# Performance work log

Hardware: AMD Instinct MI355X
Metric: run time of the kernel (lower is better)

The kernel has to match this reference:

```python
import jax, jax.numpy as jnp
import numpy as np

QK_DIM = 64
V_DIM = 64
NUM_Q_HEADS = 16
NUM_KV_HEADS = 4
GROUP = NUM_Q_HEADS // NUM_KV_HEADS
SCALE = 1.0 / (QK_DIM ** 0.5)


def setup_inputs() -> dict:
    key = jax.random.key(0)
    kq, kk, kv = jax.random.split(key, 3)
    B, S = 2, 2048
    Q = jax.random.normal(kq, (B, S, NUM_Q_HEADS * QK_DIM), dtype=jnp.float32)
    K = jax.random.normal(kk, (B, S, NUM_KV_HEADS * QK_DIM), dtype=jnp.float32)
    V = jax.random.normal(kv, (B, S, NUM_KV_HEADS * V_DIM), dtype=jnp.float32)
    # causal mask, [B, 1, S, S]; 0 entries are masked (matches masked_fill(mask == 0, -inf))
    mask = jnp.broadcast_to(jnp.tril(jnp.ones((S, S), dtype=jnp.int32))[None, None], (B, 1, S, S))
    return {"Q": Q, "K": K, "V": V, "mask": mask}


def reference(Q, K, V, mask):
    B, S, _ = Q.shape
    # [B, Hkv, g, S, d]
    Qg = Q.reshape(B, S, NUM_Q_HEADS, QK_DIM).transpose(0, 2, 1, 3).reshape(B, NUM_KV_HEADS, GROUP, S, QK_DIM)
    Kh = K.reshape(B, S, NUM_KV_HEADS, QK_DIM).transpose(0, 2, 1, 3)  # [B, Hkv, S, d]
    Vh = V.reshape(B, S, NUM_KV_HEADS, V_DIM).transpose(0, 2, 1, 3)   # [B, Hkv, S, dv]
    # scores: [B, Hkv, g, S, S]
    scores = jnp.einsum('bhgsd,bhtd->bhgst', Qg, Kh) * SCALE
    scores = jnp.where(mask[:, None] == 0, -jnp.inf, scores)
    probs = jax.nn.softmax(scores, axis=-1)
    # dropout p=0.0 -> identity (eval semantics)
    out = jnp.einsum('bhgst,bhtv->bhgsv', probs, Vh)
    return out
```

## Files before the change

### kernel.cpp

```cpp
#include <hip/hip_runtime.h>
#include <hip/hip_bf16.h>

typedef unsigned short u16;
typedef unsigned int u32;
typedef __attribute__((ext_vector_type(8))) short bf16x8;
typedef __attribute__((ext_vector_type(16))) float f32x16;

#define S_LEN 2048
#define NHQ   16
#define NHKV  4
#define HD    64
#define KVSTR (NHKV*HD)
#define QSTR  (NHQ*HD)
#define TILE_U16 4096
#define HEAD_U16 (32*TILE_U16)
#define VT_OFF   (8*HEAD_U16)
#define QSCALE 0.18033688011112042f
#define MBIAS (-24.0f)

__device__ __forceinline__ u32 cvt2(float lo, float hi) {
    __hip_bfloat162 hh = __float22bfloat162_rn(make_float2(lo, hi));
    union { __hip_bfloat162 h; u32 u; } c; c.h = hh; return c.u;
}
__device__ __forceinline__ u16 cvt1(float x) {
    __hip_bfloat16 hh = __float2bfloat16(x);
    union { __hip_bfloat16 h; u16 u; } c; c.h = hh; return c.u;
}

typedef __attribute__((address_space(3))) u32 lds_u32;
typedef __attribute__((address_space(1))) const u32 glb_u32;
__device__ __forceinline__ void gld_lds16(const void* g, void* l) {
    __builtin_amdgcn_global_load_lds((glb_u32*)g, (lds_u32*)l, 16, 0, 0);
}

__global__ __launch_bounds__(256)
void prep_kv(const float* __restrict__ Kp, const float* __restrict__ Vp,
             u16* __restrict__ WS)
{
    const int bid = blockIdx.x;
    const int t   = bid & 31;
    const int kvh = (bid >> 5) & 3;
    const int b   = bid >> 7;
    const int tid = threadIdx.x;

    u16* kt = WS + (size_t)bid * TILE_U16;
    u16* vt = WS + VT_OFF + (size_t)bid * TILE_U16;

    {
        const int r   = tid >> 2;
        const int c16 = (tid & 3) << 4;
        const float* kg = Kp + ((size_t)(b*S_LEN) + t*64 + r) * KVSTR + kvh*HD + c16;
        const float4 a  = *(const float4*)(kg);
        const float4 b4 = *(const float4*)(kg + 4);
        const float4 c  = *(const float4*)(kg + 8);
        const float4 d  = *(const float4*)(kg + 12);
        const int swz = (r & 7) << 3;
        *(uint4*)(kt + r*64 + (c16 ^ swz)) =
            make_uint4(cvt2(a.x,a.y), cvt2(a.z,a.w), cvt2(b4.x,b4.y), cvt2(b4.z,b4.w));
        *(uint4*)(kt + r*64 + ((c16+8) ^ swz)) =
            make_uint4(cvt2(c.x,c.y), cvt2(c.z,c.w), cvt2(d.x,d.y), cvt2(d.z,d.w));
    }
    {
        const int kv  = tid & 63;
        const int dv0 = (tid >> 6) << 4;
        const float* vg = Vp + ((size_t)(b*S_LEN) + t*64 + kv) * KVSTR + kvh*HD + dv0;
        float4 vv[4];
        vv[0] = *(const float4*)(vg);
        vv[1] = *(const float4*)(vg + 4);
        vv[2] = *(const float4*)(vg + 8);
        vv[3] = *(const float4*)(vg + 12);
        #pragma unroll
        for (int g4 = 0; g4 < 4; ++g4) {
            const int dv = dv0 + g4*4;
            vt[(dv+0)*64 + (kv ^ (((dv+0)&7)<<3))] = cvt1(vv[g4].x);
            vt[(dv+1)*64 + (kv ^ (((dv+1)&7)<<3))] = cvt1(vv[g4].y);
            vt[(dv+2)*64 + (kv ^ (((dv+2)&7)<<3))] = cvt1(vv[g4].z);
            vt[(dv+3)*64 + (kv ^ (((dv+3)&7)<<3))] = cvt1(vv[g4].w);
        }
    }
}

__global__ __launch_bounds__(512, 4)
void gqa_fwd_kernel(const float* __restrict__ Qp, const u16* __restrict__ WS,
                    float* __restrict__ Op)
{
    __shared__ __align__(16) char smem[65536];
    float* Mo = (float*)smem;
    float* Ml = (float*)(smem + 34816);

    const int tid  = threadIdx.x;
    const int w    = tid >> 6;
    const int lane = tid & 63;
    const int q31  = lane & 31;
    const int h    = lane >> 5;

    const int g  = __popc(w) & 1;
    const int rg = w >> 1;
    const int dr = rg >> 1;

    const int bid  = blockIdx.x;
    const int head = bid & 31;
    const int j    = bid >> 5;
    const int qt   = (j < 8) ? (15 - j) : (j - 8);
    const int kvh  = head & 3;
    const int b    = (head >> 2) & 1;
    const int qh   = kvh * 4 + (head >> 3);

    const u16* Kt = WS + (size_t)(b*4 + kvh) * HEAD_U16;
    const u16* Vt = WS + VT_OFF + (size_t)(b*4 + kvh) * HEAD_U16;

    const int qrow = qt*128 + rg*32 + q31;
    const int qcmp = (rg & 1)*32 + q31;
    const float* qp = Qp + ((size_t)b * S_LEN + qrow) * QSTR + qh*HD;
    float*       ob = Op + ((size_t)(b*NHQ + qh) * S_LEN + qrow) * HD;

    const size_t gofs = (size_t)rg*2048 + (size_t)lane*16;

    const int rswz = (q31 & 7) << 3;

    {
        const char* kg = (const char*)(Kt + (size_t)g*TILE_U16) + gofs;
        const char* vg = (const char*)(Vt + (size_t)g*TILE_U16) + gofs;
        char* kl = smem + (g*2 + 0)*8192 + rg*2048;
        char* vl = smem + 32768 + (g*2 + 0)*8192 + rg*2048;
        gld_lds16(kg, kl);  gld_lds16(kg + 1024, kl + 1024);
        gld_lds16(vg, vl);  gld_lds16(vg + 1024, vl + 1024);
    }

    bf16x8 qf[4];
    #pragma unroll
    for (int ks = 0; ks < 4; ++ks) {
        const int d = ks*16 + h*8;
        const float4 x = *(const float4*)(qp + d);
        const float4 y = *(const float4*)(qp + d + 4);
        union { u32 u[4]; bf16x8 v; } t4;
        t4.u[0] = cvt2(x.x*QSCALE, x.y*QSCALE);
        t4.u[1] = cvt2(x.z*QSCALE, x.w*QSCALE);
        t4.u[2] = cvt2(y.x*QSCALE, y.y*QSCALE);
        t4.u[3] = cvt2(y.z*QSCALE, y.w*QSCALE);
        qf[ks] = t4.v;
    }

    f32x16 MB;
    #pragma unroll
    for (int i = 0; i < 16; ++i) MB[i] = MBIAS;

    f32x16 oacc0, oacc1;
    #pragma unroll
    for (int i = 0; i < 16; ++i) { oacc0[i] = 0.f; oacc1[i] = 0.f; }
    float l_p = 0.f;

    __syncthreads();

    for (int p = 0; p <= qt; ++p) {
        const int bf = p & 1;
        if (p < qt) {
            const char* kg = (const char*)(Kt + (size_t)(2*(p+1)+g)*TILE_U16) + gofs;
            const char* vg = (const char*)(Vt + (size_t)(2*(p+1)+g)*TILE_U16) + gofs;
            char* kl = smem + (g*2 + (bf^1))*8192 + rg*2048;
            char* vl = smem + 32768 + (g*2 + (bf^1))*8192 + rg*2048;
            gld_lds16(kg, kl);  gld_lds16(kg + 1024, kl + 1024);
            gld_lds16(vg, vl);  gld_lds16(vg + 1024, vl + 1024);
        }

        if (p < qt || !(dr == 0 && g == 1)) {
            const u16* Kb = (const u16*)(smem + (g*2 + bf)*8192);
            const u16* Vb = (const u16*)(smem + 32768 + (g*2 + bf)*8192);

            f32x16 s0, s1;
            __builtin_amdgcn_s_setprio(1);
            {
                const int col = (h*8) ^ rswz;
                bf16x8 k0 = *(const bf16x8*)(&Kb[q31*64 + col]);
                bf16x8 k1 = *(const bf16x8*)(&Kb[(32 + q31)*64 + col]);
                s0 = __builtin_amdgcn_mfma_f32_32x32x16_bf16(k0, qf[0], MB, 0, 0, 0);
                s1 = __builtin_amdgcn_mfma_f32_32x32x16_bf16(k1, qf[0], MB, 0, 0, 0);
            }
            #pragma unroll
            for (int ks = 1; ks < 4; ++ks) {
                const int col = (ks*16 + h*8) ^ rswz;
                bf16x8 k0 = *(const bf16x8*)(&Kb[q31*64 + col]);
                bf16x8 k1 = *(const bf16x8*)(&Kb[(32 + q31)*64 + col]);
                s0 = __builtin_amdgcn_mfma_f32_32x32x16_bf16(k0, qf[ks], s0, 0, 0, 0);
                s1 = __builtin_amdgcn_mfma_f32_32x32x16_bf16(k1, qf[ks], s1, 0, 0, 0);
            }
            __builtin_amdgcn_s_setprio(0);

            if (p == qt && g == dr) {
                #pragma unroll
                for (int r = 0; r < 16; ++r) {
                    const int kvl = (r & 3) + 8*(r >> 2) + 4*h;
                    if (kvl > qcmp)      s0[r] = -1e30f;
                    if (kvl + 32 > qcmp) s1[r] = -1e30f;
                }
            }

            float ps0 = 0.f, ps1 = 0.f;
            #pragma unroll
            for (int r = 0; r < 16; ++r) {
                const float p0 = __builtin_amdgcn_exp2f(s0[r]);
                const float p1 = __builtin_amdgcn_exp2f(s1[r]);
                s0[r] = p0; ps0 += p0;
                s1[r] = p1; ps1 += p1;
            }
            l_p += ps0 + ps1;

            u32 Aw[8], Bw[8];
            #pragma unroll
            for (int m = 0; m < 4; ++m) {
                Aw[m]   = cvt2(s0[m*4+0], s0[m*4+1]);
                Bw[m]   = cvt2(s0[m*4+2], s0[m*4+3]);
                Aw[4+m] = cvt2(s1[m*4+0], s1[m*4+1]);
                Bw[4+m] = cvt2(s1[m*4+2], s1[m*4+3]);
            }

            __builtin_amdgcn_s_setprio(1);
            #pragma unroll
            for (int c = 0; c < 4; ++c) {
                u32 w0 = Aw[2*c], w2 = Aw[2*c+1];
                u32 w1 = Bw[2*c], w3 = Bw[2*c+1];
                asm("v_permlane32_swap_b32 %0, %1" : "+v"(w0), "+v"(w2));
                asm("v_permlane32_swap_b32 %0, %1" : "+v"(w1), "+v"(w3));
                union { u32 u[4]; bf16x8 v; } pu;
                pu.u[0] = w0; pu.u[1] = w1; pu.u[2] = w2; pu.u[3] = w3;
                const int col = (c*16 + h*8) ^ rswz;
                bf16x8 v0 = *(const bf16x8*)(&Vb[q31*64 + col]);
                bf16x8 v1 = *(const bf16x8*)(&Vb[(32 + q31)*64 + col]);
                oacc0 = __builtin_amdgcn_mfma_f32_32x32x16_bf16(v0, pu.v, oacc0, 0, 0, 0);
                oacc1 = __builtin_amdgcn_mfma_f32_32x32x16_bf16(v1, pu.v, oacc1, 0, 0, 0);
            }
            __builtin_amdgcn_s_setprio(0);
        }

        __syncthreads();
    }

    l_p += __shfl_xor(l_p, 32);
    if (g == 1) {
        float* mo = Mo + ((size_t)rg*32 + q31) * 68;
        #pragma unroll
        for (int k2 = 0; k2 < 4; ++k2) {
            *(float4*)(mo + 8*k2 + 4*h) =
                make_float4(oacc0[4*k2], oacc0[4*k2+1], oacc0[4*k2+2], oacc0[4*k2+3]);
            *(float4*)(mo + 32 + 8*k2 + 4*h) =
                make_float4(oacc1[4*k2], oacc1[4*k2+1], oacc1[4*k2+2], oacc1[4*k2+3]);
        }
        if (h == 0) Ml[rg*32 + q31] = l_p;
    }
    __syncthreads();
    if (g == 0) {
        const float inv = 1.0f / (l_p + Ml[rg*32 + q31]);
        const float* mo = Mo + ((size_t)rg*32 + q31) * 68;
        #pragma unroll
        for (int k2 = 0; k2 < 4; ++k2) {
            const float4 p0 = *(const float4*)(mo + 8*k2 + 4*h);
            const float4 p1 = *(const float4*)(mo + 32 + 8*k2 + 4*h);
            float4 o;
            o.x = (oacc0[4*k2+0] + p0.x)*inv;
            o.y = (oacc0[4*k2+1] + p0.y)*inv;
            o.z = (oacc0[4*k2+2] + p0.z)*inv;
            o.w = (oacc0[4*k2+3] + p0.w)*inv;
            *(float4*)(ob + 8*k2 + 4*h) = o;
            o.x = (oacc1[4*k2+0] + p1.x)*inv;
            o.y = (oacc1[4*k2+1] + p1.y)*inv;
            o.z = (oacc1[4*k2+2] + p1.z)*inv;
            o.w = (oacc1[4*k2+3] + p1.w)*inv;
            *(float4*)(ob + 32 + 8*k2 + 4*h) = o;
        }
    }
}

extern "C" void kernel_launch(void* const* d_in, const int* in_sizes, int n_in,
                              void* d_out, int out_size, void* d_ws, size_t ws_size,
                              hipStream_t stream) {
    const float* Q = (const float*)d_in[0];
    const float* K = (const float*)d_in[1];
    const float* V = (const float*)d_in[2];
    float* O  = (float*)d_out;
    u16*  WS = (u16*)d_ws;

    prep_kv<<<dim3(256), dim3(256), 0, stream>>>(K, V, WS);
    gqa_fwd_kernel<<<dim3(512), dim3(512), 0, stream>>>(Q, WS, O);
}
```

Before: 40.18 us.

## Load K fragments directly from global memory instead of staging through LDS

K tiles are no longer double-buffered in shared memory. Each wave reads its bf16 K fragments straight from the global workspace into registers at the start of each iteration, and the K swizzle in the prep kernel is removed to match. Shared memory drops to about 35 KB and only V is staged via LDS, while launch bounds change from 4 to 2 blocks per SM, which allows more registers per thread. The risk is exposed global/L2 load latency on the K path, since these loads are not prefetched a tile ahead and wait directly before the MFMAs.

```diff
diff --git a/kernel.cpp b/kernel.cpp
--- a/kernel.cpp
+++ b/kernel.cpp
@@ -54,10 +54,9 @@
         const float4 b4 = *(const float4*)(kg + 4);
         const float4 c  = *(const float4*)(kg + 8);
         const float4 d  = *(const float4*)(kg + 12);
-        const int swz = (r & 7) << 3;
-        *(uint4*)(kt + r*64 + (c16 ^ swz)) =
+        *(uint4*)(kt + r*64 + c16) =
             make_uint4(cvt2(a.x,a.y), cvt2(a.z,a.w), cvt2(b4.x,b4.y), cvt2(b4.z,b4.w));
-        *(uint4*)(kt + r*64 + ((c16+8) ^ swz)) =
+        *(uint4*)(kt + r*64 + c16 + 8) =
             make_uint4(cvt2(c.x,c.y), cvt2(c.z,c.w), cvt2(d.x,d.y), cvt2(d.z,d.w));
     }
     {
@@ -80,11 +79,11 @@
     }
 }
 
-__global__ __launch_bounds__(512, 4)
+__global__ __launch_bounds__(512, 2)
 void gqa_fwd_kernel(const float* __restrict__ Qp, const u16* __restrict__ WS,
                     float* __restrict__ Op)
 {
-    __shared__ __align__(16) char smem[65536];
+    __shared__ __align__(16) char smem[35840];
     float* Mo = (float*)smem;
     float* Ml = (float*)(smem + 34816);
 
@@ -116,14 +115,12 @@
 
     const size_t gofs = (size_t)rg*2048 + (size_t)lane*16;
 
+    const int kofs0 = q31*64 + h*8;
     const int rswz = (q31 & 7) << 3;
 
     {
-        const char* kg = (const char*)(Kt + (size_t)g*TILE_U16) + gofs;
         const char* vg = (const char*)(Vt + (size_t)g*TILE_U16) + gofs;
-        char* kl = smem + (g*2 + 0)*8192 + rg*2048;
-        char* vl = smem + 32768 + (g*2 + 0)*8192 + rg*2048;
-        gld_lds16(kg, kl);  gld_lds16(kg + 1024, kl + 1024);
+        char* vl = smem + (g*2 + 0)*8192 + rg*2048;
         gld_lds16(vg, vl);  gld_lds16(vg + 1024, vl + 1024);
     }
 
@@ -154,35 +151,35 @@
 
     for (int p = 0; p <= qt; ++p) {
         const int bf = p & 1;
+        const bool compute = (p < qt) || !(dr == 0 && g == 1);
+
+        bf16x8 k0[4], k1[4];
+        if (compute) {
+            const u16* Ktile = Kt + (size_t)(2*p + g)*TILE_U16;
+            #pragma unroll
+            for (int ks = 0; ks < 4; ++ks) {
+                k0[ks] = *(const bf16x8*)(Ktile + kofs0 + ks*16);
+                k1[ks] = *(const bf16x8*)(Ktile + kofs0 + 32*64 + ks*16);
+            }
+        }
+
         if (p < qt) {
-            const char* kg = (const char*)(Kt + (size_t)(2*(p+1)+g)*TILE_U16) + gofs;
             const char* vg = (const char*)(Vt + (size_t)(2*(p+1)+g)*TILE_U16) + gofs;
-            char* kl = smem + (g*2 + (bf^1))*8192 + rg*2048;
-            char* vl = smem + 32768 + (g*2 + (bf^1))*8192 + rg*2048;
-            gld_lds16(kg, kl);  gld_lds16(kg + 1024, kl + 1024);
+            char* vl = smem + (g*2 + (bf^1))*8192 + rg*2048;
             gld_lds16(vg, vl);  gld_lds16(vg + 1024, vl + 1024);
         }
 
-        if (p < qt || !(dr == 0 && g == 1)) {
-            const u16* Kb = (const u16*)(smem + (g*2 + bf)*8192);
-            const u16* Vb = (const u16*)(smem + 32768 + (g*2 + bf)*8192);
+        if (compute) {
+            const u16* Vb = (const u16*)(smem + (g*2 + bf)*8192);
 
             f32x16 s0, s1;
             __builtin_amdgcn_s_setprio(1);
-            {
-                const int col = (h*8) ^ rswz;
-                bf16x8 k0 = *(const bf16x8*)(&Kb[q31*64 + col]);
-                bf16x8 k1 = *(const bf16x8*)(&Kb[(32 + q31)*64 + col]);
-                s0 = __builtin_amdgcn_mfma_f32_32x32x16_bf16(k0, qf[0], MB, 0, 0, 0);
-                s1 = __builtin_amdgcn_mfma_f32_32x32x16_bf16(k1, qf[0], MB, 0, 0, 0);
-            }
+            s0 = __builtin_amdgcn_mfma_f32_32x32x16_bf16(k0[0], qf[0], MB, 0, 0, 0);
+            s1 = __builtin_amdgcn_mfma_f32_32x32x16_bf16(k1[0], qf[0], MB, 0, 0, 0);
             #pragma unroll
             for (int ks = 1; ks < 4; ++ks) {
-                const int col = (ks*16 + h*8) ^ rswz;
-                bf16x8 k0 = *(const bf16x8*)(&Kb[q31*64 + col]);
-                bf16x8 k1 = *(const bf16x8*)(&Kb[(32 + q31)*64 + col]);
-                s0 = __builtin_amdgcn_mfma_f32_32x32x16_bf16(k0, qf[ks], s0, 0, 0, 0);
-                s1 = __builtin_amdgcn_mfma_f32_32x32x16_bf16(k1, qf[ks], s1, 0, 0, 0);
+                s0 = __builtin_amdgcn_mfma_f32_32x32x16_bf16(k0[ks], qf[ks], s0, 0, 0, 0);
+                s1 = __builtin_amdgcn_mfma_f32_32x32x16_bf16(k1[ks], qf[ks], s1, 0, 0, 0);
             }
             __builtin_amdgcn_s_setprio(0);
 
```

Measured after the change: 76.04 us. 1.89x slower.

## Halve block size and process two query sub-tiles per wave to reuse K fragments

Applied to the files above, without the earlier changes.

Each block drops from 8 waves to 4, and each wave now handles two 32-row query sub-tiles (A and B) against the same K/V tile. K fragments are loaded from LDS once and fed to both QK^T MFMA chains, and V fragments are shared across both PV updates. Each wave issues twice as many global-to-LDS copies per stage. This removes redundant LDS reads and halves the thread count, at the cost of roughly doubled accumulator registers per wave, lower wave-level parallelism and new causal-mask special cases.

```diff
diff --git a/kernel.cpp b/kernel.cpp
--- a/kernel.cpp
+++ b/kernel.cpp
@@ -80,7 +80,7 @@
     }
 }
 
-__global__ __launch_bounds__(512, 4)
+__global__ __launch_bounds__(256, 2)
 void gqa_fwd_kernel(const float* __restrict__ Qp, const u16* __restrict__ WS,
                     float* __restrict__ Op)
 {
@@ -94,9 +94,8 @@
     const int q31  = lane & 31;
     const int h    = lane >> 5;
 
-    const int g  = __popc(w) & 1;
+    const int g  = w & 1;
     const int rg = w >> 1;
-    const int dr = rg >> 1;
 
     const int bid  = blockIdx.x;
     const int head = bid & 31;
@@ -109,125 +108,194 @@
     const u16* Kt = WS + (size_t)(b*4 + kvh) * HEAD_U16;
     const u16* Vt = WS + VT_OFF + (size_t)(b*4 + kvh) * HEAD_U16;
 
-    const int qrow = qt*128 + rg*32 + q31;
-    const int qcmp = (rg & 1)*32 + q31;
-    const float* qp = Qp + ((size_t)b * S_LEN + qrow) * QSTR + qh*HD;
-    float*       ob = Op + ((size_t)(b*NHQ + qh) * S_LEN + qrow) * HD;
-
-    const size_t gofs = (size_t)rg*2048 + (size_t)lane*16;
+    const int qrowA = qt*128 + rg*64 + q31;
+    const float* qpA = Qp + ((size_t)b * S_LEN + qrowA) * QSTR + qh*HD;
+    const float* qpB = qpA + (size_t)32 * QSTR;
+    float* obA = Op + ((size_t)(b*NHQ + qh) * S_LEN + qrowA) * HD;
+    float* obB = obA + 32*HD;
+
+    const size_t gofs = (size_t)rg*4096 + (size_t)lane*16;
 
     const int rswz = (q31 & 7) << 3;
 
     {
         const char* kg = (const char*)(Kt + (size_t)g*TILE_U16) + gofs;
         const char* vg = (const char*)(Vt + (size_t)g*TILE_U16) + gofs;
-        char* kl = smem + (g*2 + 0)*8192 + rg*2048;
-        char* vl = smem + 32768 + (g*2 + 0)*8192 + rg*2048;
-        gld_lds16(kg, kl);  gld_lds16(kg + 1024, kl + 1024);
-        gld_lds16(vg, vl);  gld_lds16(vg + 1024, vl + 1024);
-    }
-
-    bf16x8 qf[4];
+        char* kl = smem + (g*2 + 0)*8192 + rg*4096;
+        char* vl = smem + 32768 + (g*2 + 0)*8192 + rg*4096;
+        #pragma unroll
+        for (int r = 0; r < 4; ++r) {
+            gld_lds16(kg + r*1024, kl + r*1024);
+            gld_lds16(vg + r*1024, vl + r*1024);
+        }
+    }
+
+    bf16x8 qfA[4], qfB[4];
     #pragma unroll
     for (int ks = 0; ks < 4; ++ks) {
         const int d = ks*16 + h*8;
-        const float4 x = *(const float4*)(qp + d);
-        const float4 y = *(const float4*)(qp + d + 4);
-        union { u32 u[4]; bf16x8 v; } t4;
-        t4.u[0] = cvt2(x.x*QSCALE, x.y*QSCALE);
-        t4.u[1] = cvt2(x.z*QSCALE, x.w*QSCALE);
-        t4.u[2] = cvt2(y.x*QSCALE, y.y*QSCALE);
-        t4.u[3] = cvt2(y.z*QSCALE, y.w*QSCALE);
-        qf[ks] = t4.v;
+        {
+            const float4 x = *(const float4*)(qpA + d);
+            const float4 y = *(const float4*)(qpA + d + 4);
+            union { u32 u[4]; bf16x8 v; } t4;
+            t4.u[0] = cvt2(x.x*QSCALE, x.y*QSCALE);
+            t4.u[1] = cvt2(x.z*QSCALE, x.w*QSCALE);
+            t4.u[2] = cvt2(y.x*QSCALE, y.y*QSCALE);
+            t4.u[3] = cvt2(y.z*QSCALE, y.w*QSCALE);
+            qfA[ks] = t4.v;
+        }
+        {
+            const float4 x = *(const float4*)(qpB + d);
+            const float4 y = *(const float4*)(qpB + d + 4);
+            union { u32 u[4]; bf16x8 v; } t4;
+            t4.u[0] = cvt2(x.x*QSCALE, x.y*QSCALE);
+            t4.u[1] = cvt2(x.z*QSCALE, x.w*QSCALE);
+            t4.u[2] = cvt2(y.x*QSCALE, y.y*QSCALE);
+            t4.u[3] = cvt2(y.z*QSCALE, y.w*QSCALE);
+            qfB[ks] = t4.v;
+        }
     }
 
     f32x16 MB;
     #pragma unroll
     for (int i = 0; i < 16; ++i) MB[i] = MBIAS;
 
-    f32x16 oacc0, oacc1;
+    f32x16 oA0, oA1, oB0, oB1;
     #pragma unroll
-    for (int i = 0; i < 16; ++i) { oacc0[i] = 0.f; oacc1[i] = 0.f; }
-    float l_p = 0.f;
+    for (int i = 0; i < 16; ++i) { oA0[i]=0.f; oA1[i]=0.f; oB0[i]=0.f; oB1[i]=0.f; }
+    float lA = 0.f, lB = 0.f;
 
     __syncthreads();
 
     for (int p = 0; p <= qt; ++p) {
         const int bf = p & 1;
+        const bool compute = (p < qt) || !(rg == 0 && g == 1);
+
         if (p < qt) {
             const char* kg = (const char*)(Kt + (size_t)(2*(p+1)+g)*TILE_U16) + gofs;
             const char* vg = (const char*)(Vt + (size_t)(2*(p+1)+g)*TILE_U16) + gofs;
-            char* kl = smem + (g*2 + (bf^1))*8192 + rg*2048;
-            char* vl = smem + 32768 + (g*2 + (bf^1))*8192 + rg*2048;
-            gld_lds16(kg, kl);  gld_lds16(kg + 1024, kl + 1024);
-            gld_lds16(vg, vl);  gld_lds16(vg + 1024, vl + 1024);
-        }
-
-        if (p < qt || !(dr == 0 && g == 1)) {
+            char* kl = smem + (g*2 + (bf^1))*8192 + rg*4096;
+            char* vl = smem + 32768 + (g*2 + (bf^1))*8192 + rg*4096;
+            #pragma unroll
+            for (int r = 0; r < 4; ++r) {
+                gld_lds16(kg + r*1024, kl + r*1024);
+                gld_lds16(vg + r*1024, vl + r*1024);
+            }
+        }
+
+        if (compute) {
             const u16* Kb = (const u16*)(smem + (g*2 + bf)*8192);
             const u16* Vb = (const u16*)(smem + 32768 + (g*2 + bf)*8192);
-
-            f32x16 s0, s1;
-            __builtin_amdgcn_s_setprio(1);
+            const bool domask = (p == qt) && (g == rg);
+
+            bf16x8 k0[4], k1[4];
+            #pragma unroll
+            for (int ks = 0; ks < 4; ++ks) {
+                const int col = (ks*16 + h*8) ^ rswz;
+                k0[ks] = *(const bf16x8*)(&Kb[q31*64 + col]);
+                k1[ks] = *(const bf16x8*)(&Kb[(32 + q31)*64 + col]);
+            }
+
+            u32 AwA[8], BwA[8], AwB[8], BwB[8];
+
             {
-                const int col = (h*8) ^ rswz;
-                bf16x8 k0 = *(const bf16x8*)(&Kb[q31*64 + col]);
-                bf16x8 k1 = *(const bf16x8*)(&Kb[(32 + q31)*64 + col]);
-                s0 = __builtin_amdgcn_mfma_f32_32x32x16_bf16(k0, qf[0], MB, 0, 0, 0);
-                s1 = __builtin_amdgcn_mfma_f32_32x32x16_bf16(k1, qf[0], MB, 0, 0, 0);
-            }
-            #pragma unroll
-            for (int ks = 1; ks < 4; ++ks) {
-                const int col = (ks*16 + h*8) ^ rswz;
-                bf16x8 k0 = *(const bf16x8*)(&Kb[q31*64 + col]);
-                bf16x8 k1 = *(const bf16x8*)(&Kb[(32 + q31)*64 + col]);
-                s0 = __builtin_amdgcn_mfma_f32_32x32x16_bf16(k0, qf[ks], s0, 0, 0, 0);
-                s1 = __builtin_amdgcn_mfma_f32_32x32x16_bf16(k1, qf[ks], s1, 0, 0, 0);
-            }
-            __builtin_amdgcn_s_setprio(0);
-
-            if (p == qt && g == dr) {
+                f32x16 s0, s1;
+                __builtin_amdgcn_s_setprio(1);
+                s0 = __builtin_amdgcn_mfma_f32_32x32x16_bf16(k0[0], qfA[0], MB, 0, 0, 0);
+                s1 = __builtin_amdgcn_mfma_f32_32x32x16_bf16(k1[0], qfA[0], MB, 0, 0, 0);
+                #pragma unroll
+                for (int ks = 1; ks < 4; ++ks) {
+                    s0 = __builtin_amdgcn_mfma_f32_32x32x16_bf16(k0[ks], qfA[ks], s0, 0, 0, 0);
+                    s1 = __builtin_amdgcn_mfma_f32_32x32x16_bf16(k1[ks], qfA[ks], s1, 0, 0, 0);
+                }
+                __builtin_amdgcn_s_setprio(0);
+                if (domask) {
+                    #pragma unroll
+                    for (int r = 0; r < 16; ++r) {
+                        const int kvl = (r & 3) + 8*(r >> 2) + 4*h;
+                        if (kvl > q31) s0[r] = -1e30f;
+                        s1[r] = -1e30f;
+                    }
+                }
+                float ps0 = 0.f, ps1 = 0.f;
                 #pragma unroll
                 for (int r = 0; r < 16; ++r) {
-                    const int kvl = (r & 3) + 8*(r >> 2) + 4*h;
-                    if (kvl > qcmp)      s0[r] = -1e30f;
-                    if (kvl + 32 > qcmp) s1[r] = -1e30f;
-                }
-            }
-
-            float ps0 = 0.f, ps1 = 0.f;
-            #pragma unroll
-            for (int r = 0; r < 16; ++r) {
-                const float p0 = __builtin_amdgcn_exp2f(s0[r]);
-                const float p1 = __builtin_amdgcn_exp2f(s1[r]);
-                s0[r] = p0; ps0 += p0;
-                s1[r] = p1; ps1 += p1;
-            }
-            l_p += ps0 + ps1;
-
-            u32 Aw[8], Bw[8];
-            #pragma unroll
-            for (int m = 0; m < 4; ++m) {
-                Aw[m]   = cvt2(s0[m*4+0], s0[m*4+1]);
-                Bw[m]   = cvt2(s0[m*4+2], s0[m*4+3]);
-                Aw[4+m] = cvt2(s1[m*4+0], s1[m*4+1]);
-                Bw[4+m] = cvt2(s1[m*4+2], s1[m*4+3]);
+                    const float p0 = __builtin_amdgcn_exp2f(s0[r]);
+                    const float p1 = __builtin_amdgcn_exp2f(s1[r]);
+                    s0[r] = p0; ps0 += p0;
+                    s1[r] = p1; ps1 += p1;
+                }
+                lA += ps0 + ps1;
+                #pragma unroll
+                for (int m = 0; m < 4; ++m) {
+                    AwA[m]   = cvt2(s0[m*4+0], s0[m*4+1]);
+                    BwA[m]   = cvt2(s0[m*4+2], s0[m*4+3]);
+                    AwA[4+m] = cvt2(s1[m*4+0], s1[m*4+1]);
+                    BwA[4+m] = cvt2(s1[m*4+2], s1[m*4+3]);
+                }
+            }
+            {
+                f32x16 s0, s1;
+                __builtin_amdgcn_s_setprio(1);
+                s0 = __builtin_amdgcn_mfma_f32_32x32x16_bf16(k0[0], qfB[0], MB, 0, 0, 0);
+                s1 = __builtin_amdgcn_mfma_f32_32x32x16_bf16(k1[0], qfB[0], MB, 0, 0, 0);
+                #pragma unroll
+                for (int ks = 1; ks < 4; ++ks) {
+                    s0 = __builtin_amdgcn_mfma_f32_32x32x16_bf16(k0[ks], qfB[ks], s0, 0, 0, 0);
+                    s1 = __builtin_amdgcn_mfma_f32_32x32x16_bf16(k1[ks], qfB[ks], s1, 0, 0, 0);
+                }
+                __builtin_amdgcn_s_setprio(0);
+                if (domask) {
+                    #pragma unroll
+                    for (int r = 0; r < 16; ++r) {
+                        const int kvl = (r & 3) + 8*(r >> 2) + 4*h;
+                        if (kvl > q31) s1[r] = -1e30f;
+                    }
+                }
+                float ps0 = 0.f, ps1 = 0.f;
+                #pragma unroll
+                for (int r = 0; r < 16; ++r) {
+                    const float p0 = __builtin_amdgcn_exp2f(s0[r]);
+                    const float p1 = __builtin_amdgcn_exp2f(s1[r]);
+                    s0[r] = p0; ps0 += p0;
+                    s1[r] = p1; ps1 += p1;
+                }
+                lB += ps0 + ps1;
+                #pragma unroll
+                for (int m = 0; m < 4; ++m) {
+                    AwB[m]   = cvt2(s0[m*4+0], s0[m*4+1]);
+                    BwB[m]   = cvt2(s0[m*4+2], s0[m*4+3]);
+                    AwB[4+m] = cvt2(s1[m*4+0], s1[m*4+1]);
+                    BwB[4+m] = cvt2(s1[m*4+2], s1[m*4+3]);
+                }
             }
 
             __builtin_amdgcn_s_setprio(1);
             #pragma unroll
             for (int c = 0; c < 4; ++c) {
-                u32 w0 = Aw[2*c], w2 = Aw[2*c+1];
-                u32 w1 = Bw[2*c], w3 = Bw[2*c+1];
-                asm("v_permlane32_swap_b32 %0, %1" : "+v"(w0), "+v"(w2));
-                asm("v_permlane32_swap_b32 %0, %1" : "+v"(w1), "+v"(w3));
-                union { u32 u[4]; bf16x8 v; } pu;
-                pu.u[0] = w0; pu.u[1] = w1; pu.u[2] = w2; pu.u[3] = w3;
                 const int col = (c*16 + h*8) ^ rswz;
                 bf16x8 v0 = *(const bf16x8*)(&Vb[q31*64 + col]);
                 bf16x8 v1 = *(const bf16x8*)(&Vb[(32 + q31)*64 + col]);
-                oacc0 = __builtin_amdgcn_mfma_f32_32x32x16_bf16(v0, pu.v, oacc0, 0, 0, 0);
-                oacc1 = __builtin_amdgcn_mfma_f32_32x32x16_bf16(v1, pu.v, oacc1, 0, 0, 0);
+                {
+                    u32 w0 = AwA[2*c], w2 = AwA[2*c+1];
+                    u32 w1 = BwA[2*c], w3 = BwA[2*c+1];
+                    asm("v_permlane32_swap_b32 %0, %1" : "+v"(w0), "+v"(w2));
+                    asm("v_permlane32_swap_b32 %0, %1" : "+v"(w1), "+v"(w3));
+                    union { u32 u[4]; bf16x8 v; } pu;
+                    pu.u[0] = w0; pu.u[1] = w1; pu.u[2] = w2; pu.u[3] = w3;
+                    oA0 = __builtin_amdgcn_mfma_f32_32x32x16_bf16(v0, pu.v, oA0, 0, 0, 0);
+                    oA1 = __builtin_amdgcn_mfma_f32_32x32x16_bf16(v1, pu.v, oA1, 0, 0, 0);
+                }
+                {
+                    u32 w0 = AwB[2*c], w2 = AwB[2*c+1];
+                    u32 w1 = BwB[2*c], w3 = BwB[2*c+1];
+                    asm("v_permlane32_swap_b32 %0, %1" : "+v"(w0), "+v"(w2));
+                    asm("v_permlane32_swap_b32 %0, %1" : "+v"(w1), "+v"(w3));
+                    union { u32 u[4]; bf16x8 v; } pu;
+                    pu.u[0] = w0; pu.u[1] = w1; pu.u[2] = w2; pu.u[3] = w3;
+                    oB0 = __builtin_amdgcn_mfma_f32_32x32x16_bf16(v0, pu.v, oB0, 0, 0, 0);
+                    oB1 = __builtin_amdgcn_mfma_f32_32x32x16_bf16(v1, pu.v, oB1, 0, 0, 0);
+                }
             }
             __builtin_amdgcn_s_setprio(0);
         }
@@ -235,37 +303,55 @@
         __syncthreads();
     }
 
-    l_p += __shfl_xor(l_p, 32);
+    lA += __shfl_xor(lA, 32);
+    lB += __shfl_xor(lB, 32);
+    const int rowA = rg*64 + q31;
+    const int rowB = rowA + 32;
     if (g == 1) {
-        float* mo = Mo + ((size_t)rg*32 + q31) * 68;
+        float* moA = Mo + (size_t)rowA * 68;
+        float* moB = Mo + (size_t)rowB * 68;
         #pragma unroll
         for (int k2 = 0; k2 < 4; ++k2) {
-            *(float4*)(mo + 8*k2 + 4*h) =
-                make_float4(oacc0[4*k2], oacc0[4*k2+1], oacc0[4*k2+2], oacc0[4*k2+3]);
-            *(float4*)(mo + 32 + 8*k2 + 4*h) =
-                make_float4(oacc1[4*k2], oacc1[4*k2+1], oacc1[4*k2+2], oacc1[4*k2+3]);
-        }
-        if (h == 0) Ml[rg*32 + q31] = l_p;
+            *(float4*)(moA + 8*k2 + 4*h)      = make_float4(oA0[4*k2], oA0[4*k2+1], oA0[4*k2+2], oA0[4*k2+3]);
+            *(float4*)(moA + 32 + 8*k2 + 4*h) = make_float4(oA1[4*k2], oA1[4*k2+1], oA1[4*k2+2], oA1[4*k2+3]);
+            *(float4*)(moB + 8*k2 + 4*h)      = make_float4(oB0[4*k2], oB0[4*k2+1], oB0[4*k2+2], oB0[4*k2+3]);
+            *(float4*)(moB + 32 + 8*k2 + 4*h) = make_float4(oB1[4*k2], oB1[4*k2+1], oB1[4*k2+2], oB1[4*k2+3]);
+        }
+        if (h == 0) { Ml[rowA] = lA; Ml[rowB] = lB; }
     }
     __syncthreads();
     if (g == 0) {
-        const float inv = 1.0f / (l_p + Ml[rg*32 + q31]);
-        const float* mo = Mo + ((size_t)rg*32 + q31) * 68;
+        const float invA = 1.0f / (lA + Ml[rowA]);
+        const float invB = 1.0f / (lB + Ml[rowB]);
+        const float* moA = Mo + (size_t)rowA * 68;
+        const float* moB = Mo + (size_t)rowB * 68;
         #pragma unroll
         for (int k2 = 0; k2 < 4; ++k2) {
-            const float4 p0 = *(const float4*)(mo + 8*k2 + 4*h);
-            const float4 p1 = *(const float4*)(mo + 32 + 8*k2 + 4*h);
+            float4 pa0 = *(const float4*)(moA + 8*k2 + 4*h);
+            float4 pa1 = *(const float4*)(moA + 32 + 8*k2 + 4*h);
+            float4 pb0 = *(const float4*)(moB + 8*k2 + 4*h);
+            float4 pb1 = *(const float4*)(moB + 32 + 8*k2 + 4*h);
             float4 o;
-            o.x = (oacc0[4*k2+0] + p0.x)*inv;
-            o.y = (oacc0[4*k2+1] + p0.y)*inv;
-            o.z = (oacc0[4*k2+2] + p0.z)*inv;
-            o.w = (oacc0[4*k2+3] + p0.w)*inv;
-            *(float4*)(ob + 8*k2 + 4*h) = o;
-            o.x = (oacc1[4*k2+0] + p1.x)*inv;
-            o.y = (oacc1[4*k2+1] + p1.y)*inv;
-            o.z = (oacc1[4*k2+2] + p1.z)*inv;
-            o.w = (oacc1[4*k2+3] + p1.w)*inv;
-            *(float4*)(ob + 32 + 8*k2 + 4*h) = o;
+            o.x = (oA0[4*k2+0] + pa0.x)*invA;
+            o.y = (oA0[4*k2+1] + pa0.y)*invA;
+            o.z = (oA0[4*k2+2] + pa0.z)*invA;
+            o.w = (oA0[4*k2+3] + pa0.w)*invA;
+            *(float4*)(obA + 8*k2 + 4*h) = o;
+            o.x = (oA1[4*k2+0] + pa1.x)*invA;
+            o.y = (oA1[4*k2+1] + pa1.y)*invA;
+            o.z = (oA1[4*k2+2] + pa1.z)*invA;
+            o.w = (oA1[4*k2+3] + pa1.w)*invA;
+            *(float4*)(obA + 32 + 8*k2 + 4*h) = o;
+            o.x = (oB0[4*k2+0] + pb0.x)*invB;
+            o.y = (oB0[4*k2+1] + pb0.y)*invB;
+            o.z = (oB0[4*k2+2] + pb0.z)*invB;
+            o.w = (oB0[4*k2+3] + pb0.w)*invB;
+            *(float4*)(obB + 8*k2 + 4*h) = o;
+            o.x = (oB1[4*k2+0] + pb1.x)*invB;
+            o.y = (oB1[4*k2+1] + pb1.y)*invB;
+            o.z = (oB1[4*k2+2] + pb1.z)*invB;
+            o.w = (oB1[4*k2+3] + pb1.w)*invB;
+            *(float4*)(obB + 32 + 8*k2 + 4*h) = o;
         }
     }
 }
@@ -280,5 +366,5 @@
     u16*  WS = (u16*)d_ws;
 
     prep_kv<<<dim3(256), dim3(256), 0, stream>>>(K, V, WS);
-    gqa_fwd_kernel<<<dim3(512), dim3(512), 0, stream>>>(Q, WS, O);
-}
+    gqa_fwd_kernel<<<dim3(512), dim3(256), 0, stream>>>(Q, WS, O);
+}
```

After: 42.17 us. 1.05x slower.

## Pair causal query tiles per block and split KV four ways

Applied to the files above, without the earlier changes.

Each block now has 1024 threads and processes two query tiles in sequence, qt = 15-j and then qt = j, so the causal work per block is equal. The launch drops to 256 blocks. The KV loop is split across four wave groups instead of two, with double-buffered tiles in 128KB of dynamic LDS. The partial outputs and row sums of the three extra groups are reduced through LDS. This targets the load imbalance of causal tiles and aims to fill every CU with a single balanced block. In exchange it needs the large dynamic LDS allocation, adds a heavier cross-group reduction, and serialises the two passes within a block.

```diff
diff --git a/kernel.cpp b/kernel.cpp
--- a/kernel.cpp
+++ b/kernel.cpp
@@ -17,6 +17,9 @@
 #define VT_OFF   (8*HEAD_U16)
 #define QSCALE 0.18033688011112042f
 #define MBIAS (-24.0f)
+#define LDS_BYTES 131072
+#define V_OFF_L   65536
+#define ML_OFF    104448
 
 __device__ __forceinline__ u32 cvt2(float lo, float hi) {
     __hip_bfloat162 hh = __float22bfloat162_rn(make_float2(lo, hi));
@@ -80,13 +83,11 @@
     }
 }
 
-__global__ __launch_bounds__(512, 4)
+__global__ __launch_bounds__(1024, 4)
 void gqa_fwd_kernel(const float* __restrict__ Qp, const u16* __restrict__ WS,
                     float* __restrict__ Op)
 {
-    __shared__ __align__(16) char smem[65536];
-    float* Mo = (float*)smem;
-    float* Ml = (float*)(smem + 34816);
+    extern __shared__ __align__(16) char smem[];
 
     const int tid  = threadIdx.x;
     const int w    = tid >> 6;
@@ -94,178 +95,197 @@
     const int q31  = lane & 31;
     const int h    = lane >> 5;
 
-    const int g  = __popc(w) & 1;
-    const int rg = w >> 1;
-    const int dr = rg >> 1;
+    const int g  = (w ^ (w >> 2)) & 3;
+    const int rg = w >> 2;
 
     const int bid  = blockIdx.x;
     const int head = bid & 31;
     const int j    = bid >> 5;
-    const int qt   = (j < 8) ? (15 - j) : (j - 8);
     const int kvh  = head & 3;
     const int b    = (head >> 2) & 1;
     const int qh   = kvh * 4 + (head >> 3);
 
     const u16* Kt = WS + (size_t)(b*4 + kvh) * HEAD_U16;
     const u16* Vt = WS + VT_OFF + (size_t)(b*4 + kvh) * HEAD_U16;
-
-    const int qrow = qt*128 + rg*32 + q31;
+    const float* Qhead = Qp + (size_t)b * S_LEN * QSTR + qh*HD;
+    float*       Ohead = Op + (size_t)(b*NHQ + qh) * S_LEN * HD;
+
+    const size_t gofs = (size_t)rg*1024 + (size_t)lane*16;
+    const int    lofs = rg*1024;
+
+    const int rswz = (q31 & 7) << 3;
     const int qcmp = (rg & 1)*32 + q31;
-    const float* qp = Qp + ((size_t)b * S_LEN + qrow) * QSTR + qh*HD;
-    float*       ob = Op + ((size_t)(b*NHQ + qh) * S_LEN + qrow) * HD;
-
-    const size_t gofs = (size_t)rg*2048 + (size_t)lane*16;
-
-    const int rswz = (q31 & 7) << 3;
-
-    {
-        const char* kg = (const char*)(Kt + (size_t)g*TILE_U16) + gofs;
-        const char* vg = (const char*)(Vt + (size_t)g*TILE_U16) + gofs;
-        char* kl = smem + (g*2 + 0)*8192 + rg*2048;
-        char* vl = smem + 32768 + (g*2 + 0)*8192 + rg*2048;
-        gld_lds16(kg, kl);  gld_lds16(kg + 1024, kl + 1024);
-        gld_lds16(vg, vl);  gld_lds16(vg + 1024, vl + 1024);
-    }
-
-    bf16x8 qf[4];
-    #pragma unroll
-    for (int ks = 0; ks < 4; ++ks) {
-        const int d = ks*16 + h*8;
-        const float4 x = *(const float4*)(qp + d);
-        const float4 y = *(const float4*)(qp + d + 4);
-        union { u32 u[4]; bf16x8 v; } t4;
-        t4.u[0] = cvt2(x.x*QSCALE, x.y*QSCALE);
-        t4.u[1] = cvt2(x.z*QSCALE, x.w*QSCALE);
-        t4.u[2] = cvt2(y.x*QSCALE, y.y*QSCALE);
-        t4.u[3] = cvt2(y.z*QSCALE, y.w*QSCALE);
-        qf[ks] = t4.v;
-    }
 
     f32x16 MB;
     #pragma unroll
     for (int i = 0; i < 16; ++i) MB[i] = MBIAS;
 
-    f32x16 oacc0, oacc1;
-    #pragma unroll
-    for (int i = 0; i < 16; ++i) { oacc0[i] = 0.f; oacc1[i] = 0.f; }
-    float l_p = 0.f;
-
-    __syncthreads();
-
-    for (int p = 0; p <= qt; ++p) {
-        const int bf = p & 1;
-        if (p < qt) {
-            const char* kg = (const char*)(Kt + (size_t)(2*(p+1)+g)*TILE_U16) + gofs;
-            const char* vg = (const char*)(Vt + (size_t)(2*(p+1)+g)*TILE_U16) + gofs;
-            char* kl = smem + (g*2 + (bf^1))*8192 + rg*2048;
-            char* vl = smem + 32768 + (g*2 + (bf^1))*8192 + rg*2048;
-            gld_lds16(kg, kl);  gld_lds16(kg + 1024, kl + 1024);
-            gld_lds16(vg, vl);  gld_lds16(vg + 1024, vl + 1024);
-        }
-
-        if (p < qt || !(dr == 0 && g == 1)) {
-            const u16* Kb = (const u16*)(smem + (g*2 + bf)*8192);
-            const u16* Vb = (const u16*)(smem + 32768 + (g*2 + bf)*8192);
-
-            f32x16 s0, s1;
-            __builtin_amdgcn_s_setprio(1);
-            {
-                const int col = (h*8) ^ rswz;
-                bf16x8 k0 = *(const bf16x8*)(&Kb[q31*64 + col]);
-                bf16x8 k1 = *(const bf16x8*)(&Kb[(32 + q31)*64 + col]);
-                s0 = __builtin_amdgcn_mfma_f32_32x32x16_bf16(k0, qf[0], MB, 0, 0, 0);
-                s1 = __builtin_amdgcn_mfma_f32_32x32x16_bf16(k1, qf[0], MB, 0, 0, 0);
+    #pragma unroll 1
+    for (int pass = 0; pass < 2; ++pass) {
+        const int qt   = pass ? j : (15 - j);
+        const int nt   = 2*qt + 1;
+        const int Pmax = nt/4 + 1;
+        const int tmax = 2*qt + (rg >> 1);
+        const int qrow = qt*128 + rg*32 + q31;
+        const float* qp = Qhead + (size_t)qrow * QSTR;
+
+        bf16x8 qf[4];
+        #pragma unroll
+        for (int ks = 0; ks < 4; ++ks) {
+            const int d = ks*16 + h*8;
+            const float4 x = *(const float4*)(qp + d);
+            const float4 y = *(const float4*)(qp + d + 4);
+            union { u32 u[4]; bf16x8 v; } t4;
+            t4.u[0] = cvt2(x.x*QSCALE, x.y*QSCALE);
+            t4.u[1] = cvt2(x.z*QSCALE, x.w*QSCALE);
+            t4.u[2] = cvt2(y.x*QSCALE, y.y*QSCALE);
+            t4.u[3] = cvt2(y.z*QSCALE, y.w*QSCALE);
+            qf[ks] = t4.v;
+        }
+
+        f32x16 oacc0, oacc1;
+        #pragma unroll
+        for (int i = 0; i < 16; ++i) { oacc0[i] = 0.f; oacc1[i] = 0.f; }
+        float l_p = 0.f;
+
+        if (pass) __syncthreads();
+
+        if (g <= nt) {
+            const char* kg = (const char*)(Kt + (size_t)g*TILE_U16) + gofs;
+            const char* vg = (const char*)(Vt + (size_t)g*TILE_U16) + gofs;
+            char* kl = smem + (g*2 + 0)*8192 + lofs;
+            char* vl = smem + V_OFF_L + (g*2 + 0)*8192 + lofs;
+            gld_lds16(kg, kl);  gld_lds16(kg + 4096, kl + 4096);
+            gld_lds16(vg, vl);  gld_lds16(vg + 4096, vl + 4096);
+        }
+        __syncthreads();
+
+        for (int p = 0; p < Pmax; ++p) {
+            const int t   = 4*p + g;
+            const int buf = p & 1;
+
+            if (t + 4 <= nt) {
+                const char* kg = (const char*)(Kt + (size_t)(t+4)*TILE_U16) + gofs;
+                const char* vg = (const char*)(Vt + (size_t)(t+4)*TILE_U16) + gofs;
+                char* kl = smem + (g*2 + (buf^1))*8192 + lofs;
+                char* vl = smem + V_OFF_L + (g*2 + (buf^1))*8192 + lofs;
+                gld_lds16(kg, kl);  gld_lds16(kg + 4096, kl + 4096);
+                gld_lds16(vg, vl);  gld_lds16(vg + 4096, vl + 4096);
             }
-            #pragma unroll
-            for (int ks = 1; ks < 4; ++ks) {
-                const int col = (ks*16 + h*8) ^ rswz;
-                bf16x8 k0 = *(const bf16x8*)(&Kb[q31*64 + col]);
-                bf16x8 k1 = *(const bf16x8*)(&Kb[(32 + q31)*64 + col]);
-                s0 = __builtin_amdgcn_mfma_f32_32x32x16_bf16(k0, qf[ks], s0, 0, 0, 0);
-                s1 = __builtin_amdgcn_mfma_f32_32x32x16_bf16(k1, qf[ks], s1, 0, 0, 0);
-            }
-            __builtin_amdgcn_s_setprio(0);
-
-            if (p == qt && g == dr) {
+
+            if (t <= tmax) {
+                const u16* Kb = (const u16*)(smem + (g*2 + buf)*8192);
+                const u16* Vb = (const u16*)(smem + V_OFF_L + (g*2 + buf)*8192);
+
+                f32x16 s0, s1;
+                __builtin_amdgcn_s_setprio(1);
+                {
+                    const int col = (h*8) ^ rswz;
+                    bf16x8 k0 = *(const bf16x8*)(&Kb[q31*64 + col]);
+                    bf16x8 k1 = *(const bf16x8*)(&Kb[(32 + q31)*64 + col]);
+                    s0 = __builtin_amdgcn_mfma_f32_32x32x16_bf16(k0, qf[0], MB, 0, 0, 0);
+                    s1 = __builtin_amdgcn_mfma_f32_32x32x16_bf16(k1, qf[0], MB, 0, 0, 0);
+                }
+                #pragma unroll
+                for (int ks = 1; ks < 4; ++ks) {
+                    const int col = (ks*16 + h*8) ^ rswz;
+                    bf16x8 k0 = *(const bf16x8*)(&Kb[q31*64 + col]);
+                    bf16x8 k1 = *(const bf16x8*)(&Kb[(32 + q31)*64 + col]);
+                    s0 = __builtin_amdgcn_mfma_f32_32x32x16_bf16(k0, qf[ks], s0, 0, 0, 0);
+                    s1 = __builtin_amdgcn_mfma_f32_32x32x16_bf16(k1, qf[ks], s1, 0, 0, 0);
+                }
+                __builtin_amdgcn_s_setprio(0);
+
+                if (t == tmax) {
+                    #pragma unroll
+                    for (int r = 0; r < 16; ++r) {
+                        const int kvl = (r & 3) + 8*(r >> 2) + 4*h;
+                        if (kvl > qcmp)      s0[r] = -1e30f;
+                        if (kvl + 32 > qcmp) s1[r] = -1e30f;
+                    }
+                }
+
+                float ps0 = 0.f, ps1 = 0.f;
                 #pragma unroll
                 for (int r = 0; r < 16; ++r) {
-                    const int kvl = (r & 3) + 8*(r >> 2) + 4*h;
-                    if (kvl > qcmp)      s0[r] = -1e30f;
-                    if (kvl + 32 > qcmp) s1[r] = -1e30f;
-                }
+                    const float p0 = __builtin_amdgcn_exp2f(s0[r]);
+                    const float p1 = __builtin_amdgcn_exp2f(s1[r]);
+                    s0[r] = p0; ps0 += p0;
+                    s1[r] = p1; ps1 += p1;
+                }
+                l_p += ps0 + ps1;
+
+                u32 Aw[8], Bw[8];
+                #pragma unroll
+                for (int m = 0; m < 4; ++m) {
+                    Aw[m]   = cvt2(s0[m*4+0], s0[m*4+1]);
+                    Bw[m]   = cvt2(s0[m*4+2], s0[m*4+3]);
+                    Aw[4+m] = cvt2(s1[m*4+0], s1[m*4+1]);
+                    Bw[4+m] = cvt2(s1[m*4+2], s1[m*4+3]);
+                }
+
+                __builtin_amdgcn_s_setprio(1);
+                #pragma unroll
+                for (int c = 0; c < 4; ++c) {
+                    u32 w0 = Aw[2*c], w2 = Aw[2*c+1];
+                    u32 w1 = Bw[2*c], w3 = Bw[2*c+1];
+                    asm("v_permlane32_swap_b32 %0, %1" : "+v"(w0), "+v"(w2));
+                    asm("v_permlane32_swap_b32 %0, %1" : "+v"(w1), "+v"(w3));
+                    union { u32 u[4]; bf16x8 v; } pu;
+                    pu.u[0] = w0; pu.u[1] = w1; pu.u[2] = w2; pu.u[3] = w3;
+                    const int col = (c*16 + h*8) ^ rswz;
+                    bf16x8 v0 = *(const bf16x8*)(&Vb[q31*64 + col]);
+                    bf16x8 v1 = *(const bf16x8*)(&Vb[(32 + q31)*64 + col]);
+                    oacc0 = __builtin_amdgcn_mfma_f32_32x32x16_bf16(v0, pu.v, oacc0, 0, 0, 0);
+                    oacc1 = __builtin_amdgcn_mfma_f32_32x32x16_bf16(v1, pu.v, oacc1, 0, 0, 0);
+                }
+                __builtin_amdgcn_s_setprio(0);
             }
 
-            float ps0 = 0.f, ps1 = 0.f;
+            __syncthreads();
+        }
+
+        l_p += __shfl_xor(l_p, 32);
+        const int row = rg*32 + q31;
+        if (g != 0) {
+            float* mo = (float*)(smem + (g-1)*34816) + (size_t)row * 68;
             #pragma unroll
-            for (int r = 0; r < 16; ++r) {
-                const float p0 = __builtin_amdgcn_exp2f(s0[r]);
-                const float p1 = __builtin_amdgcn_exp2f(s1[r]);
-                s0[r] = p0; ps0 += p0;
-                s1[r] = p1; ps1 += p1;
+            for (int k2 = 0; k2 < 4; ++k2) {
+                *(float4*)(mo + 8*k2 + 4*h) =
+                    make_float4(oacc0[4*k2], oacc0[4*k2+1], oacc0[4*k2+2], oacc0[4*k2+3]);
+                *(float4*)(mo + 32 + 8*k2 + 4*h) =
+                    make_float4(oacc1[4*k2], oacc1[4*k2+1], oacc1[4*k2+2], oacc1[4*k2+3]);
             }
-            l_p += ps0 + ps1;
-
-            u32 Aw[8], Bw[8];
+            if (h == 0) ((float*)(smem + ML_OFF))[(g-1)*128 + row] = l_p;
+        }
+        __syncthreads();
+        if (g == 0) {
+            const float* Mlp = (const float*)(smem + ML_OFF);
+            const float inv = 1.0f / (l_p + Mlp[row] + Mlp[128 + row] + Mlp[256 + row]);
+            const float* m0 = (const float*)(smem + 0*34816) + (size_t)row * 68;
+            const float* m1 = (const float*)(smem + 1*34816) + (size_t)row * 68;
+            const float* m2 = (const float*)(smem + 2*34816) + (size_t)row * 68;
+            float* ob = Ohead + (size_t)qrow * HD;
             #pragma unroll
-            for (int m = 0; m < 4; ++m) {
-                Aw[m]   = cvt2(s0[m*4+0], s0[m*4+1]);
-                Bw[m]   = cvt2(s0[m*4+2], s0[m*4+3]);
-                Aw[4+m] = cvt2(s1[m*4+0], s1[m*4+1]);
-                Bw[4+m] = cvt2(s1[m*4+2], s1[m*4+3]);
+            for (int k2 = 0; k2 < 4; ++k2) {
+                const float4 a0 = *(const float4*)(m0 + 8*k2 + 4*h);
+                const float4 b0 = *(const float4*)(m1 + 8*k2 + 4*h);
+                const float4 c0 = *(const float4*)(m2 + 8*k2 + 4*h);
+                const float4 a1 = *(const float4*)(m0 + 32 + 8*k2 + 4*h);
+                const float4 b1 = *(const float4*)(m1 + 32 + 8*k2 + 4*h);
+                const float4 c1 = *(const float4*)(m2 + 32 + 8*k2 + 4*h);
+                float4 o;
+                o.x = (oacc0[4*k2+0] + a0.x + b0.x + c0.x) * inv;
+                o.y = (oacc0[4*k2+1] + a0.y + b0.y + c0.y) * inv;
+                o.z = (oacc0[4*k2+2] + a0.z + b0.z + c0.z) * inv;
+                o.w = (oacc0[4*k2+3] + a0.w + b0.w + c0.w) * inv;
+                *(float4*)(ob + 8*k2 + 4*h) = o;
+                o.x = (oacc1[4*k2+0] + a1.x + b1.x + c1.x) * inv;
+                o.y = (oacc1[4*k2+1] + a1.y + b1.y + c1.y) * inv;
+                o.z = (oacc1[4*k2+2] + a1.z + b1.z + c1.z) * inv;
+                o.w = (oacc1[4*k2+3] + a1.w + b1.w + c1.w) * inv;
+                *(float4*)(ob + 32 + 8*k2 + 4*h) = o;
             }
-
-            __builtin_amdgcn_s_setprio(1);
-            #pragma unroll
-            for (int c = 0; c < 4; ++c) {
-                u32 w0 = Aw[2*c], w2 = Aw[2*c+1];
-                u32 w1 = Bw[2*c], w3 = Bw[2*c+1];
-                asm("v_permlane32_swap_b32 %0, %1" : "+v"(w0), "+v"(w2));
-                asm("v_permlane32_swap_b32 %0, %1" : "+v"(w1), "+v"(w3));
-                union { u32 u[4]; bf16x8 v; } pu;
-                pu.u[0] = w0; pu.u[1] = w1; pu.u[2] = w2; pu.u[3] = w3;
-                const int col = (c*16 + h*8) ^ rswz;
-                bf16x8 v0 = *(const bf16x8*)(&Vb[q31*64 + col]);
-                bf16x8 v1 = *(const bf16x8*)(&Vb[(32 + q31)*64 + col]);
-                oacc0 = __builtin_amdgcn_mfma_f32_32x32x16_bf16(v0, pu.v, oacc0, 0, 0, 0);
-                oacc1 = __builtin_amdgcn_mfma_f32_32x32x16_bf16(v1, pu.v, oacc1, 0, 0, 0);
-            }
-            __builtin_amdgcn_s_setprio(0);
-        }
-
-        __syncthreads();
-    }
-
-    l_p += __shfl_xor(l_p, 32);
-    if (g == 1) {
-        float* mo = Mo + ((size_t)rg*32 + q31) * 68;
-        #pragma unroll
-        for (int k2 = 0; k2 < 4; ++k2) {
-            *(float4*)(mo + 8*k2 + 4*h) =
-                make_float4(oacc0[4*k2], oacc0[4*k2+1], oacc0[4*k2+2], oacc0[4*k2+3]);
-            *(float4*)(mo + 32 + 8*k2 + 4*h) =
-                make_float4(oacc1[4*k2], oacc1[4*k2+1], oacc1[4*k2+2], oacc1[4*k2+3]);
-        }
-        if (h == 0) Ml[rg*32 + q31] = l_p;
-    }
-    __syncthreads();
-    if (g == 0) {
-        const float inv = 1.0f / (l_p + Ml[rg*32 + q31]);
-        const float* mo = Mo + ((size_t)rg*32 + q31) * 68;
-        #pragma unroll
-        for (int k2 = 0; k2 < 4; ++k2) {
-            const float4 p0 = *(const float4*)(mo + 8*k2 + 4*h);
-            const float4 p1 = *(const float4*)(mo + 32 + 8*k2 + 4*h);
-            float4 o;
-            o.x = (oacc0[4*k2+0] + p0.x)*inv;
-            o.y = (oacc0[4*k2+1] + p0.y)*inv;
-            o.z = (oacc0[4*k2+2] + p0.z)*inv;
-            o.w = (oacc0[4*k2+3] + p0.w)*inv;
-            *(float4*)(ob + 8*k2 + 4*h) = o;
-            o.x = (oacc1[4*k2+0] + p1.x)*inv;
-            o.y = (oacc1[4*k2+1] + p1.y)*inv;
-            o.z = (oacc1[4*k2+2] + p1.z)*inv;
-            o.w = (oacc1[4*k2+3] + p1.w)*inv;
-            *(float4*)(ob + 32 + 8*k2 + 4*h) = o;
         }
     }
 }
@@ -280,5 +300,5 @@
     u16*  WS = (u16*)d_ws;
 
     prep_kv<<<dim3(256), dim3(256), 0, stream>>>(K, V, WS);
-    gqa_fwd_kernel<<<dim3(512), dim3(512), 0, stream>>>(Q, WS, O);
-}
+    gqa_fwd_kernel<<<dim3(256), dim3(1024), LDS_BYTES, stream>>>(Q, WS, O);
+}
```

Measured after the change: 50.83 us. 26.5% more time.
